# Kernel optimization log

Measured on AMD Instinct MI355X. Metric: run time of the kernel, lower is better.

Reference implementation:

```python
import jax, jax.numpy as jnp
import numpy as np

B, M, IN, HID, A = 4096, 64, 3, 128, 64
D = 50.0                       # waveguide_bound
H_CONST = 5.0
PMAX = 10.0 ** (30 / 10 - 3)   # = 1.0 (30 dBm in Watts)
C_LIGHT = 3.0e8
FC = 6.0e9
DELTA_MIN = (C_LIGHT / FC) / 2.0  # 0.025
ALPHA = 0.2                    # LeakyReLU slope


def setup_inputs() -> dict:
    key = jax.random.key(0)
    ks = jax.random.split(key, 9)
    s = lambda k, sh: (jax.random.normal(k, sh, jnp.float32) * 0.1)
    return {
        "users": jax.random.normal(ks[0], (B, M, IN), jnp.float32),
        "W1": s(ks[1], (IN, HID)),    # GAT layer 1 projection (applied as h @ W)
        "a1": s(ks[2], (2 * HID,)),   # GAT layer 1 attention vector
        "W2": s(ks[3], (HID, HID)),   # GAT layer 2 projection
        "a2": s(ks[4], (2 * HID,)),
        "mw1": s(ks[5], (HID, 32)),   # MLP Linear(hidden, 32)
        "mb1": jnp.zeros((32,), jnp.float32),
        "mw2": s(ks[6], (32, 2 * A)), # MLP Linear(32, 2*num_antennas)
        "mb2": jnp.zeros((2 * A,), jnp.float32),
    }


def gat_layer(h, W, a):
    # Wh: [B, M, d]
    Wh = h @ W
    d = W.shape[1]
    # e[b,i,j] = leakyrelu( cat(Wh_i, Wh_j) . a ) = leakyrelu( Wh_i.a[:d] + Wh_j.a[d:] )
    si = Wh @ a[:d]          # [B, M]
    sj = Wh @ a[d:]          # [B, M]
    e = jax.nn.leaky_relu(si[:, :, None] + sj[:, None, :], ALPHA)  # [B, M, M]
    attn = jax.nn.softmax(e, axis=-1)  # softmax over neighbors j (dropout p=0 -> identity)
    h_prime = jnp.einsum('bij,bjd->bid', attn, Wh)
    return jax.nn.elu(h_prime)


def reference(users, W1, a1, W2, a2, mw1, mb1, mw2, mb2):
    h = gat_layer(users, W1, a1)
    h = gat_layer(h, W2, a2)
    pooled = jnp.max(h, axis=1)                      # [B, hidden]
    readout = jax.nn.relu(pooled @ mw1 + mb1) @ mw2 + mb2  # [B, 2A]
    raw_delta, raw_power = readout[:, :A], readout[:, A:]
    eps = 1e-6
    raw_delta = jax.nn.relu(raw_delta) + eps
    raw_power = jax.nn.relu(raw_power) + eps
    Bmax = 2.0 * D - (A - 1) * DELTA_MIN
    delta = Bmax * raw_delta / (jnp.sum(raw_delta, axis=1, keepdims=True) + eps)
    power = PMAX * raw_power / (jnp.sum(raw_power, axis=1, keepdims=True) + eps)
    return power, delta
```

## Files before the change

kernel.cpp:

```cpp
#include <hip/hip_runtime.h>

#define NBATCH 4096
#define OUT2 (NBATCH * 64)

typedef _Float16 f16;
typedef __attribute__((ext_vector_type(8))) _Float16 f16x8;
typedef __attribute__((ext_vector_type(4))) _Float16 f16x4;
typedef __attribute__((ext_vector_type(4))) float f32x4;

__device__ __forceinline__ float lrelu(float x) { return x > 0.0f ? x : 0.2f * x; }
__device__ __forceinline__ float elu1(float x)  { return x > 0.0f ? x : __expf(x) - 1.0f; }

__global__ void prep(const float* __restrict__ W2, const float* __restrict__ W1,
                     const float* __restrict__ a1, const float* __restrict__ a2,
                     f16* __restrict__ w2b, float* __restrict__ w1a, f16* __restrict__ w2ab) {
    const int flat = blockIdx.x * 256 + threadIdx.x;
    const int slot = flat >> 3, j = flat & 7;
    const int F2T = slot >> 8, kf = (slot >> 6) & 3, ln = slot & 63;
    const int lq = ln >> 4, lr = ln & 15;
    w2b[flat] = (f16)W2[(kf * 32 + lq * 8 + j) * 128 + F2T * 16 + lr];
    if (flat < 2048) {
        const int ks = flat >> 9, ln2 = (flat >> 3) & 63, jj = flat & 7;
        const int k = ks * 32 + ((ln2 >> 4) & 3) * 8 + jj;
        const int n = ln2 & 15;
        float v = 0.f;
        if (n < 2) {
            const float* av = a2 + n * 128;
            for (int f2 = 0; f2 < 128; ++f2) v = fmaf(W2[k * 128 + f2], av[f2], v);
        }
        w2ab[flat] = (f16)v;
    }
    if (flat >= 16381) {
        const int c = flat - 16381;
        float si = 0.f, sj = 0.f;
        for (int f = 0; f < 128; ++f) {
            const float w = W1[c * 128 + f];
            si = fmaf(w, a1[f], si);
            sj = fmaf(w, a1[128 + f], sj);
        }
        w1a[c] = si; w1a[3 + c] = sj;
    }
}

__global__ __launch_bounds__(64, 3)
void gat_kernel(const float* __restrict__ users,
                const float* __restrict__ W1,
                const f16* __restrict__ w2b,
                const float* __restrict__ w1a,
                const f16* __restrict__ w2ab,
                const float* __restrict__ mw1,
                const float* __restrict__ mb1,
                const float* __restrict__ mw2,
                const float* __restrict__ mb2,
                float* __restrict__ out)
{
    const int b = blockIdx.x;
    const int lane = threadIdx.x;
    const int lr = lane & 15;
    const int lq = lane >> 4;

    __shared__ __align__(16) char smem[17536];
    f16*   sMain = (f16*)smem;
    float* sSi   = (float*)(smem + 16384);
    float* sSj   = (float*)(smem + 16640);
    float* sPool = (float*)(smem + 16896);
    float* sHid  = (float*)(smem + 17408);

    {
        const float* u = users + b * 192;
        const float x = u[lane * 3], y = u[lane * 3 + 1], z = u[lane * 3 + 2];
        sSi[lane] = fmaf(x, w1a[0], fmaf(y, w1a[1], z * w1a[2]));
        sSj[lane] = fmaf(x, w1a[3], fmaf(y, w1a[4], z * w1a[5]));
    }
    __syncthreads();

    f16x8 ap[4][2];
    float inv1[4];
    {
        float sjv[16];
        *(float4*)&sjv[0]  = *(const float4*)&sSj[lq * 8];
        *(float4*)&sjv[4]  = *(const float4*)&sSj[lq * 8 + 4];
        *(float4*)&sjv[8]  = *(const float4*)&sSj[32 + lq * 8];
        *(float4*)&sjv[12] = *(const float4*)&sSj[32 + lq * 8 + 4];
        #pragma unroll
        for (int mt = 0; mt < 4; ++mt) {
            const float si = sSi[mt * 16 + lr];
            float lsum = 0.f;
            #pragma unroll
            for (int jj = 0; jj < 8; ++jj) {
                float p = __expf(lrelu(si + sjv[jj]));
                f16 ph = (f16)p; lsum += (float)ph; ap[mt][0][jj] = ph;
                p = __expf(lrelu(si + sjv[8 + jj]));
                ph = (f16)p; lsum += (float)ph; ap[mt][1][jj] = ph;
            }
            lsum += __shfl_xor(lsum, 16, 64);
            lsum += __shfl_xor(lsum, 32, 64);
            inv1[mt] = 1.0f / lsum;
        }
    }

    f16x8 af2[2];
    #pragma unroll
    for (int ks = 0; ks < 2; ++ks) {
        #pragma unroll
        for (int jj = 0; jj < 8; ++jj) {
            const int node = ks * 32 + lq * 8 + jj;
            af2[ks][jj] = (lr < 3) ? (f16)users[b * 192 + node * 3 + lr] : (f16)0.f;
        }
    }
    f32x4 d1[4];
    #pragma unroll
    for (int nt = 0; nt < 4; ++nt) {
        d1[nt] = (f32x4){0.f, 0.f, 0.f, 0.f};
        d1[nt] = __builtin_amdgcn_mfma_f32_16x16x32_f16(af2[0], ap[nt][0], d1[nt], 0, 0, 0);
        d1[nt] = __builtin_amdgcn_mfma_f32_16x16x32_f16(af2[1], ap[nt][1], d1[nt], 0, 0, 0);
    }
    f16x8 bfr[4];
    #pragma unroll
    for (int nt = 0; nt < 4; ++nt) {
        const float c0 = __shfl(d1[nt][0], lr, 64);
        const float c1 = __shfl(d1[nt][1], lr, 64);
        const float c2 = __shfl(d1[nt][2], lr, 64);
        #pragma unroll
        for (int jj = 0; jj < 8; ++jj) bfr[nt][jj] = (f16)0.f;
        if (lq == 0) {
            bfr[nt][0] = (f16)c0; bfr[nt][1] = (f16)c1; bfr[nt][2] = (f16)c2;
        }
    }

    f16x8 hf[4][4];
    #pragma unroll
    for (int h = 0; h < 2; ++h) {
        __syncthreads();
        #pragma unroll
        for (int ftl = 0; ftl < 4; ++ftl) {
            f16x8 af3;
            #pragma unroll
            for (int jj = 0; jj < 8; ++jj) af3[jj] = (f16)0.f;
            if (lq == 0) {
                #pragma unroll
                for (int jj = 0; jj < 3; ++jj)
                    af3[jj] = (f16)W1[jj * 128 + (h * 4 + ftl) * 16 + lr];
            }
            #pragma unroll
            for (int nt = 0; nt < 4; ++nt) {
                f32x4 acc = (f32x4){0.f, 0.f, 0.f, 0.f};
                acc = __builtin_amdgcn_mfma_f32_16x16x32_f16(af3, bfr[nt], acc, 0, 0, 0);
                f16x4 hv;
                #pragma unroll
                for (int r = 0; r < 4; ++r) hv[r] = (f16)elu1(acc[r] * inv1[nt]);
                const int n = nt * 16 + lr;
                const int g = 2 * ftl + (lq >> 1);
                *(f16x4*)&sMain[n * 64 + ((g ^ (n & 7)) << 3) + ((lq & 1) * 4)] = hv;
            }
        }
        __syncthreads();
        #pragma unroll
        for (int nt = 0; nt < 4; ++nt) {
            const int n = nt * 16 + lr;
            #pragma unroll
            for (int ksl = 0; ksl < 2; ++ksl)
                hf[nt][h * 2 + ksl] =
                    *(const f16x8*)&sMain[n * 64 + (((ksl * 4 + lq) ^ (n & 7)) << 3)];
        }
    }

    {
        f32x4 sacc[4];
        #pragma unroll
        for (int mt = 0; mt < 4; ++mt) sacc[mt] = (f32x4){0.f, 0.f, 0.f, 0.f};
        #pragma unroll
        for (int ks = 0; ks < 4; ++ks) {
            f16x8 bsw = *(const f16x8*)(w2ab + (ks * 64 + lane) * 8);
            #pragma unroll
            for (int mt = 0; mt < 4; ++mt)
                sacc[mt] = __builtin_amdgcn_mfma_f32_16x16x32_f16(hf[mt][ks], bsw, sacc[mt], 0, 0, 0);
        }
        if (lr < 2) {
            float* dst = (lr == 0) ? sSi : sSj;
            #pragma unroll
            for (int mt = 0; mt < 4; ++mt) {
                #pragma unroll
                for (int r = 0; r < 4; ++r)
                    dst[mt * 16 + lq * 4 + r] = sacc[mt][r];
            }
        }
        __syncthreads();
    }

    #pragma unroll
    for (int h = 0; h < 2; ++h) {
        #pragma unroll
        for (int f2t = 0; f2t < 4; ++f2t) {
            f16x8 bw2[4];
            #pragma unroll
            for (int kf = 0; kf < 4; ++kf)
                bw2[kf] = *(const f16x8*)(w2b + (((h * 4 + f2t) * 4 + kf) * 64 + lane) * 8);
            #pragma unroll
            for (int ntile = 0; ntile < 4; ++ntile) {
                f32x4 acc = (f32x4){0.f, 0.f, 0.f, 0.f};
                #pragma unroll
                for (int kf = 0; kf < 4; ++kf)
                    acc = __builtin_amdgcn_mfma_f32_16x16x32_f16(hf[ntile][kf], bw2[kf], acc, 0, 0, 0);
                const int fl = h * 64 + f2t * 16 + lr;
                const int g = ntile * 2 + (lq >> 1);
                f16x4 hv;
                #pragma unroll
                for (int r = 0; r < 4; ++r) hv[r] = (f16)acc[r];
                *(f16x4*)&sMain[fl * 64 + ((g ^ (fl & 7)) << 3) + ((lq & 1) * 4)] = hv;
            }
        }
    }
    __syncthreads();

    {
        f16x8 bp[4][2];
        float inv2[4];
        {
            float sjv[16];
            *(float4*)&sjv[0]  = *(const float4*)&sSj[lq * 8];
            *(float4*)&sjv[4]  = *(const float4*)&sSj[lq * 8 + 4];
            *(float4*)&sjv[8]  = *(const float4*)&sSj[32 + lq * 8];
            *(float4*)&sjv[12] = *(const float4*)&sSj[32 + lq * 8 + 4];
            #pragma unroll
            for (int mt = 0; mt < 4; ++mt) {
                const float si = sSi[mt * 16 + lr];
                float lsum = 0.f;
                #pragma unroll
                for (int jj = 0; jj < 8; ++jj) {
                    float p = __expf(lrelu(si + sjv[jj]));
                    f16 ph = (f16)p; lsum += (float)ph; bp[mt][0][jj] = ph;
                    p = __expf(lrelu(si + sjv[8 + jj]));
                    ph = (f16)p; lsum += (float)ph; bp[mt][1][jj] = ph;
                }
                lsum += __shfl_xor(lsum, 16, 64);
                lsum += __shfl_xor(lsum, 32, 64);
                inv2[mt] = 1.0f / lsum;
            }
        }

        #pragma unroll
        for (int ftl = 0; ftl < 8; ++ftl) {
            const int fl = ftl * 16 + lr;
            f16x8 b0 = *(const f16x8*)&sMain[fl * 64 + ((lq ^ (fl & 7)) << 3)];
            f16x8 b1 = *(const f16x8*)&sMain[fl * 64 + (((4 + lq) ^ (fl & 7)) << 3)];
            f32x4 mx4 = (f32x4){-1e30f, -1e30f, -1e30f, -1e30f};
            #pragma unroll
            for (int mt = 0; mt < 4; ++mt) {
                f32x4 acc = (f32x4){0.f, 0.f, 0.f, 0.f};
                acc = __builtin_amdgcn_mfma_f32_16x16x32_f16(b0, bp[mt][0], acc, 0, 0, 0);
                acc = __builtin_amdgcn_mfma_f32_16x16x32_f16(b1, bp[mt][1], acc, 0, 0, 0);
                #pragma unroll
                for (int r = 0; r < 4; ++r)
                    mx4[r] = fmaxf(mx4[r], acc[r] * inv2[mt]);
            }
            #pragma unroll
            for (int m = 1; m < 16; m <<= 1) {
                #pragma unroll
                for (int r = 0; r < 4; ++r)
                    mx4[r] = fmaxf(mx4[r], __shfl_xor(mx4[r], m, 64));
            }
            if (lr == 0) {
                float4 pv;
                pv.x = elu1(mx4[0]); pv.y = elu1(mx4[1]);
                pv.z = elu1(mx4[2]); pv.w = elu1(mx4[3]);
                *(float4*)&sPool[ftl * 16 + lq * 4] = pv;
            }
        }
    }
    __syncthreads();

    {
        const int o = lane & 31, hh = lane >> 5;
        float s = 0.f;
        #pragma unroll 8
        for (int kk = 0; kk < 64; ++kk) {
            const int c = hh * 64 + kk;
            s = fmaf(sPool[c], mw1[c * 32 + o], s);
        }
        s += __shfl_xor(s, 32, 64);
        s = fmaxf(s + mb1[o], 0.0f);
        if (lane < 32) sHid[lane] = s;
    }
    __syncthreads();
    {
        float sA = mb2[lane], sB = mb2[64 + lane];
        #pragma unroll 8
        for (int q = 0; q < 32; ++q) {
            const float hq = sHid[q];
            sA = fmaf(hq, mw2[q * 128 + lane], sA);
            sB = fmaf(hq, mw2[q * 128 + 64 + lane], sB);
        }
        const float rA = fmaxf(sA, 0.0f) + 1e-6f;
        const float rB = fmaxf(sB, 0.0f) + 1e-6f;
        float sumA = rA, sumB = rB;
        #pragma unroll
        for (int m = 1; m < 64; m <<= 1) {
            sumA += __shfl_xor(sumA, m, 64);
            sumB += __shfl_xor(sumB, m, 64);
        }
        out[b * 64 + lane]        = rB / (sumB + 1e-6f);
        out[OUT2 + b * 64 + lane] = 98.425f * rA / (sumA + 1e-6f);
    }
}

extern "C" void kernel_launch(void* const* d_in, const int* in_sizes, int n_in,
                              void* d_out, int out_size, void* d_ws, size_t ws_size,
                              hipStream_t stream) {
    const float* users = (const float*)d_in[0];
    const float* W1    = (const float*)d_in[1];
    const float* a1    = (const float*)d_in[2];
    const float* W2    = (const float*)d_in[3];
    const float* a2    = (const float*)d_in[4];
    const float* mw1   = (const float*)d_in[5];
    const float* mb1   = (const float*)d_in[6];
    const float* mw2   = (const float*)d_in[7];
    const float* mb2   = (const float*)d_in[8];
    float* out = (float*)d_out;

    f16*   w2b  = (f16*)d_ws;
    float* w1a  = (float*)((char*)d_ws + 32768);
    f16*   w2ab = (f16*)((char*)d_ws + 32800);

    prep<<<64, 256, 0, stream>>>(W2, W1, a1, a2, w2b, w1a, w2ab);
    gat_kernel<<<NBATCH, 64, 0, stream>>>(users, W1, w2b, w1a, w2ab,
                                          mw1, mb1, mw2, mb2, out);
}
```

Before: 121.5 us.

## Process two batch graphs per wavefront to amortize weight loads

```diff
diff --git a/kernel.cpp b/kernel.cpp
--- a/kernel.cpp
+++ b/kernel.cpp
@@ -42,7 +42,7 @@
     }
 }
 
-__global__ __launch_bounds__(64, 3)
+__global__ __launch_bounds__(64, 2)
 void gat_kernel(const float* __restrict__ users,
                 const float* __restrict__ W1,
                 const f16* __restrict__ w2b,
@@ -54,34 +54,39 @@
                 const float* __restrict__ mb2,
                 float* __restrict__ out)
 {
-    const int b = blockIdx.x;
+    const int b0 = blockIdx.x * 2;
     const int lane = threadIdx.x;
     const int lr = lane & 15;
     const int lq = lane >> 4;
 
-    __shared__ __align__(16) char smem[17536];
+    __shared__ __align__(16) char smem[18688];
     f16*   sMain = (f16*)smem;
-    float* sSi   = (float*)(smem + 16384);
-    float* sSj   = (float*)(smem + 16640);
-    float* sPool = (float*)(smem + 16896);
-    float* sHid  = (float*)(smem + 17408);
-
-    {
-        const float* u = users + b * 192;
+    float* sSiA  = (float*)(smem + 16384);
+    float* sSjA  = (float*)(smem + 16896);
+    float* sPoolA= (float*)(smem + 17408);
+    float* sHidA = (float*)(smem + 18432);
+
+    #pragma unroll
+    for (int g = 0; g < 2; ++g) {
+        const float* u = users + (b0 + g) * 192;
         const float x = u[lane * 3], y = u[lane * 3 + 1], z = u[lane * 3 + 2];
-        sSi[lane] = fmaf(x, w1a[0], fmaf(y, w1a[1], z * w1a[2]));
-        sSj[lane] = fmaf(x, w1a[3], fmaf(y, w1a[4], z * w1a[5]));
+        sSiA[g * 64 + lane] = fmaf(x, w1a[0], fmaf(y, w1a[1], z * w1a[2]));
+        sSjA[g * 64 + lane] = fmaf(x, w1a[3], fmaf(y, w1a[4], z * w1a[5]));
     }
     __syncthreads();
 
-    f16x8 ap[4][2];
-    float inv1[4];
-    {
+    f16x8 bfr[2][4];
+    float inv1[2][4];
+    #pragma unroll
+    for (int g = 0; g < 2; ++g) {
+        const float* sSi = sSiA + g * 64;
+        const float* sSj = sSjA + g * 64;
         float sjv[16];
         *(float4*)&sjv[0]  = *(const float4*)&sSj[lq * 8];
         *(float4*)&sjv[4]  = *(const float4*)&sSj[lq * 8 + 4];
         *(float4*)&sjv[8]  = *(const float4*)&sSj[32 + lq * 8];
         *(float4*)&sjv[12] = *(const float4*)&sSj[32 + lq * 8 + 4];
+        f16x8 ap[4][2];
         #pragma unroll
         for (int mt = 0; mt < 4; ++mt) {
             const float si = sSi[mt * 16 + lr];
@@ -95,40 +100,34 @@
             }
             lsum += __shfl_xor(lsum, 16, 64);
             lsum += __shfl_xor(lsum, 32, 64);
-            inv1[mt] = 1.0f / lsum;
-        }
-    }
-
-    f16x8 af2[2];
-    #pragma unroll
-    for (int ks = 0; ks < 2; ++ks) {
-        #pragma unroll
-        for (int jj = 0; jj < 8; ++jj) {
-            const int node = ks * 32 + lq * 8 + jj;
-            af2[ks][jj] = (lr < 3) ? (f16)users[b * 192 + node * 3 + lr] : (f16)0.f;
-        }
-    }
-    f32x4 d1[4];
-    #pragma unroll
-    for (int nt = 0; nt < 4; ++nt) {
-        d1[nt] = (f32x4){0.f, 0.f, 0.f, 0.f};
-        d1[nt] = __builtin_amdgcn_mfma_f32_16x16x32_f16(af2[0], ap[nt][0], d1[nt], 0, 0, 0);
-        d1[nt] = __builtin_amdgcn_mfma_f32_16x16x32_f16(af2[1], ap[nt][1], d1[nt], 0, 0, 0);
-    }
-    f16x8 bfr[4];
-    #pragma unroll
-    for (int nt = 0; nt < 4; ++nt) {
-        const float c0 = __shfl(d1[nt][0], lr, 64);
-        const float c1 = __shfl(d1[nt][1], lr, 64);
-        const float c2 = __shfl(d1[nt][2], lr, 64);
-        #pragma unroll
-        for (int jj = 0; jj < 8; ++jj) bfr[nt][jj] = (f16)0.f;
-        if (lq == 0) {
-            bfr[nt][0] = (f16)c0; bfr[nt][1] = (f16)c1; bfr[nt][2] = (f16)c2;
-        }
-    }
-
-    f16x8 hf[4][4];
+            inv1[g][mt] = 1.0f / lsum;
+        }
+        f16x8 af2[2];
+        #pragma unroll
+        for (int ks = 0; ks < 2; ++ks) {
+            #pragma unroll
+            for (int jj = 0; jj < 8; ++jj) {
+                const int node = ks * 32 + lq * 8 + jj;
+                af2[ks][jj] = (lr < 3) ? (f16)users[(b0 + g) * 192 + node * 3 + lr] : (f16)0.f;
+            }
+        }
+        #pragma unroll
+        for (int nt = 0; nt < 4; ++nt) {
+            f32x4 d1 = (f32x4){0.f, 0.f, 0.f, 0.f};
+            d1 = __builtin_amdgcn_mfma_f32_16x16x32_f16(af2[0], ap[nt][0], d1, 0, 0, 0);
+            d1 = __builtin_amdgcn_mfma_f32_16x16x32_f16(af2[1], ap[nt][1], d1, 0, 0, 0);
+            const float c0 = __shfl(d1[0], lr, 64);
+            const float c1 = __shfl(d1[1], lr, 64);
+            const float c2 = __shfl(d1[2], lr, 64);
+            #pragma unroll
+            for (int jj = 0; jj < 8; ++jj) bfr[g][nt][jj] = (f16)0.f;
+            if (lq == 0) {
+                bfr[g][nt][0] = (f16)c0; bfr[g][nt][1] = (f16)c1; bfr[g][nt][2] = (f16)c2;
+            }
+        }
+    }
+
+    f16x8 hf[2][4][4];
     #pragma unroll
     for (int h = 0; h < 2; ++h) {
         __syncthreads();
@@ -143,77 +142,92 @@
                     af3[jj] = (f16)W1[jj * 128 + (h * 4 + ftl) * 16 + lr];
             }
             #pragma unroll
+            for (int g = 0; g < 2; ++g) {
+                #pragma unroll
+                for (int nt = 0; nt < 4; ++nt) {
+                    f32x4 acc = (f32x4){0.f, 0.f, 0.f, 0.f};
+                    acc = __builtin_amdgcn_mfma_f32_16x16x32_f16(af3, bfr[g][nt], acc, 0, 0, 0);
+                    f16x4 hv;
+                    #pragma unroll
+                    for (int r = 0; r < 4; ++r) hv[r] = (f16)elu1(acc[r] * inv1[g][nt]);
+                    const int n = nt * 16 + lr;
+                    const int gg = 2 * ftl + (lq >> 1);
+                    *(f16x4*)&sMain[g * 4096 + n * 64 + ((gg ^ (n & 7)) << 3) + ((lq & 1) * 4)] = hv;
+                }
+            }
+        }
+        __syncthreads();
+        #pragma unroll
+        for (int g = 0; g < 2; ++g) {
+            #pragma unroll
             for (int nt = 0; nt < 4; ++nt) {
-                f32x4 acc = (f32x4){0.f, 0.f, 0.f, 0.f};
-                acc = __builtin_amdgcn_mfma_f32_16x16x32_f16(af3, bfr[nt], acc, 0, 0, 0);
-                f16x4 hv;
-                #pragma unroll
-                for (int r = 0; r < 4; ++r) hv[r] = (f16)elu1(acc[r] * inv1[nt]);
                 const int n = nt * 16 + lr;
-                const int g = 2 * ftl + (lq >> 1);
-                *(f16x4*)&sMain[n * 64 + ((g ^ (n & 7)) << 3) + ((lq & 1) * 4)] = hv;
-            }
-        }
-        __syncthreads();
-        #pragma unroll
-        for (int nt = 0; nt < 4; ++nt) {
-            const int n = nt * 16 + lr;
-            #pragma unroll
-            for (int ksl = 0; ksl < 2; ++ksl)
-                hf[nt][h * 2 + ksl] =
-                    *(const f16x8*)&sMain[n * 64 + (((ksl * 4 + lq) ^ (n & 7)) << 3)];
+                #pragma unroll
+                for (int ksl = 0; ksl < 2; ++ksl)
+                    hf[g][nt][h * 2 + ksl] =
+                        *(const f16x8*)&sMain[g * 4096 + n * 64 + (((ksl * 4 + lq) ^ (n & 7)) << 3)];
+            }
         }
     }
 
     {
-        f32x4 sacc[4];
-        #pragma unroll
-        for (int mt = 0; mt < 4; ++mt) sacc[mt] = (f32x4){0.f, 0.f, 0.f, 0.f};
+        f32x4 sacc[2][4];
+        #pragma unroll
+        for (int g = 0; g < 2; ++g)
+            #pragma unroll
+            for (int mt = 0; mt < 4; ++mt) sacc[g][mt] = (f32x4){0.f, 0.f, 0.f, 0.f};
         #pragma unroll
         for (int ks = 0; ks < 4; ++ks) {
             f16x8 bsw = *(const f16x8*)(w2ab + (ks * 64 + lane) * 8);
             #pragma unroll
-            for (int mt = 0; mt < 4; ++mt)
-                sacc[mt] = __builtin_amdgcn_mfma_f32_16x16x32_f16(hf[mt][ks], bsw, sacc[mt], 0, 0, 0);
+            for (int g = 0; g < 2; ++g)
+                #pragma unroll
+                for (int mt = 0; mt < 4; ++mt)
+                    sacc[g][mt] = __builtin_amdgcn_mfma_f32_16x16x32_f16(hf[g][mt][ks], bsw, sacc[g][mt], 0, 0, 0);
         }
         if (lr < 2) {
-            float* dst = (lr == 0) ? sSi : sSj;
-            #pragma unroll
-            for (int mt = 0; mt < 4; ++mt) {
-                #pragma unroll
-                for (int r = 0; r < 4; ++r)
-                    dst[mt * 16 + lq * 4 + r] = sacc[mt][r];
-            }
-        }
+            #pragma unroll
+            for (int g = 0; g < 2; ++g) {
+                float* dst = (lr == 0) ? (sSiA + g * 64) : (sSjA + g * 64);
+                #pragma unroll
+                for (int mt = 0; mt < 4; ++mt)
+                    #pragma unroll
+                    for (int r = 0; r < 4; ++r)
+                        dst[mt * 16 + lq * 4 + r] = sacc[g][mt][r];
+            }
+        }
+    }
+
+    #pragma unroll
+    for (int g = 0; g < 2; ++g) {
         __syncthreads();
-    }
-
-    #pragma unroll
-    for (int h = 0; h < 2; ++h) {
-        #pragma unroll
-        for (int f2t = 0; f2t < 4; ++f2t) {
-            f16x8 bw2[4];
-            #pragma unroll
-            for (int kf = 0; kf < 4; ++kf)
-                bw2[kf] = *(const f16x8*)(w2b + (((h * 4 + f2t) * 4 + kf) * 64 + lane) * 8);
-            #pragma unroll
-            for (int ntile = 0; ntile < 4; ++ntile) {
-                f32x4 acc = (f32x4){0.f, 0.f, 0.f, 0.f};
+        #pragma unroll
+        for (int h = 0; h < 2; ++h) {
+            #pragma unroll
+            for (int f2t = 0; f2t < 4; ++f2t) {
+                f16x8 bw2[4];
                 #pragma unroll
                 for (int kf = 0; kf < 4; ++kf)
-                    acc = __builtin_amdgcn_mfma_f32_16x16x32_f16(hf[ntile][kf], bw2[kf], acc, 0, 0, 0);
-                const int fl = h * 64 + f2t * 16 + lr;
-                const int g = ntile * 2 + (lq >> 1);
-                f16x4 hv;
-                #pragma unroll
-                for (int r = 0; r < 4; ++r) hv[r] = (f16)acc[r];
-                *(f16x4*)&sMain[fl * 64 + ((g ^ (fl & 7)) << 3) + ((lq & 1) * 4)] = hv;
-            }
-        }
-    }
-    __syncthreads();
-
-    {
+                    bw2[kf] = *(const f16x8*)(w2b + (((h * 4 + f2t) * 4 + kf) * 64 + lane) * 8);
+                #pragma unroll
+                for (int ntile = 0; ntile < 4; ++ntile) {
+                    f32x4 acc = (f32x4){0.f, 0.f, 0.f, 0.f};
+                    #pragma unroll
+                    for (int kf = 0; kf < 4; ++kf)
+                        acc = __builtin_amdgcn_mfma_f32_16x16x32_f16(hf[g][ntile][kf], bw2[kf], acc, 0, 0, 0);
+                    const int fl = h * 64 + f2t * 16 + lr;
+                    const int gg = ntile * 2 + (lq >> 1);
+                    f16x4 hv;
+                    #pragma unroll
+                    for (int r = 0; r < 4; ++r) hv[r] = (f16)acc[r];
+                    *(f16x4*)&sMain[fl * 64 + ((gg ^ (fl & 7)) << 3) + ((lq & 1) * 4)] = hv;
+                }
+            }
+        }
+        __syncthreads();
+
+        const float* sSi = sSiA + g * 64;
+        const float* sSj = sSjA + g * 64;
         f16x8 bp[4][2];
         float inv2[4];
         {
@@ -238,18 +252,17 @@
                 inv2[mt] = 1.0f / lsum;
             }
         }
-
         #pragma unroll
         for (int ftl = 0; ftl < 8; ++ftl) {
             const int fl = ftl * 16 + lr;
-            f16x8 b0 = *(const f16x8*)&sMain[fl * 64 + ((lq ^ (fl & 7)) << 3)];
-            f16x8 b1 = *(const f16x8*)&sMain[fl * 64 + (((4 + lq) ^ (fl & 7)) << 3)];
+            f16x8 bh0 = *(const f16x8*)&sMain[fl * 64 + ((lq ^ (fl & 7)) << 3)];
+            f16x8 bh1 = *(const f16x8*)&sMain[fl * 64 + (((4 + lq) ^ (fl & 7)) << 3)];
             f32x4 mx4 = (f32x4){-1e30f, -1e30f, -1e30f, -1e30f};
             #pragma unroll
             for (int mt = 0; mt < 4; ++mt) {
                 f32x4 acc = (f32x4){0.f, 0.f, 0.f, 0.f};
-                acc = __builtin_amdgcn_mfma_f32_16x16x32_f16(b0, bp[mt][0], acc, 0, 0, 0);
-                acc = __builtin_amdgcn_mfma_f32_16x16x32_f16(b1, bp[mt][1], acc, 0, 0, 0);
+                acc = __builtin_amdgcn_mfma_f32_16x16x32_f16(bh0, bp[mt][0], acc, 0, 0, 0);
+                acc = __builtin_amdgcn_mfma_f32_16x16x32_f16(bh1, bp[mt][1], acc, 0, 0, 0);
                 #pragma unroll
                 for (int r = 0; r < 4; ++r)
                     mx4[r] = fmaxf(mx4[r], acc[r] * inv2[mt]);
@@ -264,7 +277,7 @@
                 float4 pv;
                 pv.x = elu1(mx4[0]); pv.y = elu1(mx4[1]);
                 pv.z = elu1(mx4[2]); pv.w = elu1(mx4[3]);
-                *(float4*)&sPool[ftl * 16 + lq * 4] = pv;
+                *(float4*)&sPoolA[g * 128 + ftl * 16 + lq * 4] = pv;
             }
         }
     }
@@ -272,35 +285,46 @@
 
     {
         const int o = lane & 31, hh = lane >> 5;
-        float s = 0.f;
+        float s0 = 0.f, s1 = 0.f;
         #pragma unroll 8
         for (int kk = 0; kk < 64; ++kk) {
             const int c = hh * 64 + kk;
-            s = fmaf(sPool[c], mw1[c * 32 + o], s);
-        }
-        s += __shfl_xor(s, 32, 64);
-        s = fmaxf(s + mb1[o], 0.0f);
-        if (lane < 32) sHid[lane] = s;
+            const float w = mw1[c * 32 + o];
+            s0 = fmaf(sPoolA[c], w, s0);
+            s1 = fmaf(sPoolA[128 + c], w, s1);
+        }
+        s0 += __shfl_xor(s0, 32, 64);
+        s1 += __shfl_xor(s1, 32, 64);
+        const float bb = mb1[o];
+        if (lane < 32) {
+            sHidA[lane] = fmaxf(s0 + bb, 0.0f);
+            sHidA[32 + lane] = fmaxf(s1 + bb, 0.0f);
+        }
     }
     __syncthreads();
     {
-        float sA = mb2[lane], sB = mb2[64 + lane];
+        const float mbA = mb2[lane], mbB = mb2[64 + lane];
+        float sA0 = mbA, sB0 = mbB, sA1 = mbA, sB1 = mbB;
         #pragma unroll 8
         for (int q = 0; q < 32; ++q) {
-            const float hq = sHid[q];
-            sA = fmaf(hq, mw2[q * 128 + lane], sA);
-            sB = fmaf(hq, mw2[q * 128 + 64 + lane], sB);
-        }
-        const float rA = fmaxf(sA, 0.0f) + 1e-6f;
-        const float rB = fmaxf(sB, 0.0f) + 1e-6f;
-        float sumA = rA, sumB = rB;
+            const float wA = mw2[q * 128 + lane];
+            const float wB = mw2[q * 128 + 64 + lane];
+            const float h0 = sHidA[q], h1 = sHidA[32 + q];
+            sA0 = fmaf(h0, wA, sA0);  sB0 = fmaf(h0, wB, sB0);
+            sA1 = fmaf(h1, wA, sA1);  sB1 = fmaf(h1, wB, sB1);
+        }
+        float rA0 = fmaxf(sA0, 0.0f) + 1e-6f, rB0 = fmaxf(sB0, 0.0f) + 1e-6f;
+        float rA1 = fmaxf(sA1, 0.0f) + 1e-6f, rB1 = fmaxf(sB1, 0.0f) + 1e-6f;
+        float uA0 = rA0, uB0 = rB0, uA1 = rA1, uB1 = rB1;
         #pragma unroll
         for (int m = 1; m < 64; m <<= 1) {
-            sumA += __shfl_xor(sumA, m, 64);
-            sumB += __shfl_xor(sumB, m, 64);
-        }
-        out[b * 64 + lane]        = rB / (sumB + 1e-6f);
-        out[OUT2 + b * 64 + lane] = 98.425f * rA / (sumA + 1e-6f);
+            uA0 += __shfl_xor(uA0, m, 64);  uB0 += __shfl_xor(uB0, m, 64);
+            uA1 += __shfl_xor(uA1, m, 64);  uB1 += __shfl_xor(uB1, m, 64);
+        }
+        out[b0 * 64 + lane]              = rB0 / (uB0 + 1e-6f);
+        out[OUT2 + b0 * 64 + lane]       = 98.425f * rA0 / (uA0 + 1e-6f);
+        out[(b0 + 1) * 64 + lane]        = rB1 / (uB1 + 1e-6f);
+        out[OUT2 + (b0 + 1) * 64 + lane] = 98.425f * rA1 / (uA1 + 1e-6f);
     }
 }
 
@@ -323,6 +347,6 @@
     f16*   w2ab = (f16*)((char*)d_ws + 32800);
 
     prep<<<64, 256, 0, stream>>>(W2, W1, a1, a2, w2b, w1a, w2ab);
-    gat_kernel<<<NBATCH, 64, 0, stream>>>(users, W1, w2b, w1a, w2ab,
-                                          mw1, mb1, mw2, mb2, out);
+    gat_kernel<<<NBATCH / 2, 64, 0, stream>>>(users, W1, w2b, w1a, w2ab,
+                                              mw1, mb1, mw2, mb2, out);
 }
```

Result: faster. 112.8 us (-7.2%).
